# Kernel tuning notes

Hardware: AMD Instinct MI355X
Metric: run time of the kernel (lower is better)

## Reference

```python
import jax, jax.numpy as jnp
import numpy as np

NUM_TAGS = 64
SEQ_LEN = 512
BATCH = 512


def setup_inputs() -> dict:
    key = jax.random.key(0)
    k1, k2, k3, k4, k5 = jax.random.split(key, 5)
    emissions = jax.random.normal(k1, (SEQ_LEN, BATCH, NUM_TAGS), dtype=jnp.float32)
    tags = jax.random.randint(k2, (SEQ_LEN, BATCH), 0, NUM_TAGS, dtype=jnp.int32)
    mask = jnp.ones((SEQ_LEN, BATCH), dtype=jnp.int32)
    start_transitions = jax.random.uniform(k3, (NUM_TAGS,), dtype=jnp.float32)
    end_transitions = jax.random.uniform(k4, (NUM_TAGS,), dtype=jnp.float32)
    transitions = jax.random.uniform(k5, (NUM_TAGS, NUM_TAGS), dtype=jnp.float32)
    return {
        "emissions": emissions,
        "tags": tags,
        "mask": mask,
        "start_transitions": start_transitions,
        "end_transitions": end_transitions,
        "transitions": transitions,
    }


def _compute_score(emissions, tags, mask, start_transitions, end_transitions, transitions):
    # emissions: (S,B,T), tags/mask: (S,B)
    seq_length, batch_size = tags.shape
    maskf = mask.astype(jnp.float32)
    barange = jnp.arange(batch_size)
    # emission scores for gold tags at every step: (S,B)
    emit = jnp.take_along_axis(emissions, tags[:, :, None], axis=2)[:, :, 0]
    # transition scores between consecutive gold tags: (S-1,B)
    trans = transitions[tags[:-1], tags[1:]]
    score = start_transitions[tags[0]] + emit[0]
    score = score + ((trans + emit[1:]) * maskf[1:]).sum(axis=0)
    seq_ends = mask.astype(jnp.int32).sum(axis=0) - 1  # (B,)
    last_tags = tags[seq_ends, barange]
    score = score + end_transitions[last_tags]
    return score  # (B,)


def _compute_normalizer(emissions, mask, start_transitions, end_transitions, transitions):
    # sequential forward-algorithm scan over time
    score0 = start_transitions + emissions[0]  # (B,T)

    def step(score, inp):
        em, m = inp  # em: (B,T), m: (B,)
        # (B,Tprev,Tnext) logsumexp over Tprev
        next_score = jax.nn.logsumexp(
            score[:, :, None] + transitions[None, :, :] + em[:, None, :], axis=1
        )
        score = jnp.where(m[:, None].astype(bool), next_score, score)
        return score, None

    score, _ = jax.lax.scan(step, score0, (emissions[1:], mask[1:]))
    return jax.nn.logsumexp(score + end_transitions, axis=1)  # (B,)


def reference(emissions, tags, mask, start_transitions, end_transitions, transitions):
    numerator = _compute_score(emissions, tags, mask, start_transitions, end_transitions, transitions)
    denominator = _compute_normalizer(emissions, mask, start_transitions, end_transitions, transitions)
    llh = numerator - denominator
    return llh.sum()  # reduction='sum'
```

## Files before the change

### kernel.cpp

```cpp
#include <hip/hip_runtime.h>

#define T   512
#define B   512
#define NT  64
#define QS  16
#define NQ  (T / QS)
#define RING 4

typedef _Float16 h2 __attribute__((ext_vector_type(2)));

__device__ __forceinline__ float rflf(float x) {
    return __uint_as_float(__builtin_amdgcn_readfirstlane(__float_as_uint(x)));
}

__device__ __forceinline__ float dot2(h2 a, h2 b, float c) {
#if __has_builtin(__builtin_amdgcn_fdot2)
    return __builtin_amdgcn_fdot2(a, b, c, false);
#else
    return c + (float)a.x * (float)b.x + (float)a.y * (float)b.y;
#endif
}

__device__ __forceinline__ h2 bch2(int u) { return __builtin_bit_cast(h2, u); }

__global__ __launch_bounds__(64) void crf_fused(
    const float* __restrict__ emissions,
    const int*   __restrict__ tags,
    const int*   __restrict__ mask,
    const float* __restrict__ startT,
    const float* __restrict__ endT,
    const float* __restrict__ trans,
    float* __restrict__ out)
{
    const int j = threadIdx.x;

    __shared__ __align__(16) float ebuf[RING][QS][NT];

    if (blockIdx.x < B) {
        const int b = blockIdx.x;

        h2 Eh[NT / 2];
#pragma unroll
        for (int m = 0; m < NT / 2; ++m) {
            Eh[m].x = (_Float16)__expf(trans[(2 * m)     * NT + j]);
            Eh[m].y = (_Float16)__expf(trans[(2 * m + 1) * NT + j]);
        }

        const int jr = j >> 4;
        const int c0 = (j & 15) * 4;
        float4 sA[4];

        auto issue_q = [&](int g) {
#pragma unroll
            for (int k = 0; k < 4; ++k) {
                const int t = g * QS + 4 * k + jr;
                sA[k] = *(const float4*)&emissions[((size_t)t * B + b) * NT + c0];
            }
        };
        auto write_q = [&](int g) {
#pragma unroll
            for (int k = 0; k < 4; ++k) {
                float4 w;
                w.x = __expf(sA[k].x); w.y = __expf(sA[k].y);
                w.z = __expf(sA[k].z); w.w = __expf(sA[k].w);
                *(float4*)&ebuf[g & (RING - 1)][4 * k + jr][c0] = w;
            }
        };

        for (int g = 0; g < 3; ++g) { issue_q(g); write_q(g); }
        issue_q(3);

        const float e0  = emissions[(size_t)b * NT + j];
        const float sc0 = startT[j] + e0;
        const float S0  = rflf(sc0);
        float q = __expf(sc0 - S0);
        int   K = 0;

        int pk_i;
        {
            const int qi = __float_as_int(q);
            const int qo = __builtin_amdgcn_update_dpp(0, qi, 0xB1, 0xF, 0xF, true);
            pk_i = __builtin_bit_cast(int,
                    __builtin_amdgcn_cvt_pkrtz(q, __int_as_float(qo)));
        }

        float* eflat = &ebuf[0][0][0];
        int bits_prev;
        int mpre = mask[j * B + b];
        unsigned long long mbc = 0;

        {
            int u[32];
#pragma unroll
            for (int n = 0; n < 32; ++n)
                u[n] = __builtin_amdgcn_readlane(pk_i, 2 * n);
            float a[8] = {0.f, 0.f, 0.f, 0.f, 0.f, 0.f, 0.f, 0.f};
#pragma unroll
            for (int n = 0; n < 32; ++n)
                a[n & 7] = dot2(bch2(u[n]), Eh[n], a[n & 7]);
            const float p = ((a[0] + a[1]) + (a[2] + a[3]))
                          + ((a[4] + a[5]) + (a[6] + a[7]));
            bits_prev = __builtin_amdgcn_readfirstlane(__float_as_int(p));
            const int  k = ((bits_prev >> 23) & 255) - 127;
            const float r = __int_as_float((125 - k) << 23);
            const float X1 = eflat[NT + j];
            const int  m1 = mask[B + b];
            if (m1) { q = (p * X1) * r; K = k + 2; }
            const int qo = __builtin_amdgcn_update_dpp(0, __float_as_int(q),
                                                       0xB1, 0xF, 0xF, true);
            pk_i = __builtin_bit_cast(int,
                    __builtin_amdgcn_cvt_pkrtz(q, __int_as_float(qo)));
        }

        float Xc = eflat[2 * NT + j];
        float Xn = eflat[3 * NT + j];

        auto stepF = [&](int s) {
            int u[32];
#pragma unroll
            for (int n = 0; n < 32; ++n)
                u[n] = __builtin_amdgcn_readlane(pk_i, 2 * n);
            __builtin_amdgcn_sched_barrier(0);
            const int  k = ((bits_prev >> 23) & 255) - 127;
            const float r = __int_as_float((125 - k) << 23);
            K += k + 2;
            float a[8] = {0.f, 0.f, 0.f, 0.f, 0.f, 0.f, 0.f, 0.f};
#pragma unroll
            for (int n = 0; n < 32; ++n)
                a[n & 7] = dot2(bch2(u[n]), Eh[n], a[n & 7]);
            const float sXr = Xc * r;
            const float p = ((a[0] + a[1]) + (a[2] + a[3]))
                          + ((a[4] + a[5]) + (a[6] + a[7]));
            q = p * sXr;
            bits_prev = __builtin_amdgcn_readfirstlane(__float_as_int(p));
            const int qo = __builtin_amdgcn_update_dpp(0, __float_as_int(q),
                                                       0xB1, 0xF, 0xF, true);
            pk_i = __builtin_bit_cast(int,
                    __builtin_amdgcn_cvt_pkrtz(q, __int_as_float(qo)));
            Xc = Xn;
            Xn = eflat[((s + 2) & 63) * NT + j];
        };

        auto stepM = [&](int s) {
            int u[32];
#pragma unroll
            for (int n = 0; n < 32; ++n)
                u[n] = __builtin_amdgcn_readlane(pk_i, 2 * n);
            __builtin_amdgcn_sched_barrier(0);
            const int  k = ((bits_prev >> 23) & 255) - 127;
            const float r = __int_as_float((125 - k) << 23);
            const bool mc = (mbc >> (s & 63)) & 1ull;
            const float mf = mc ? 1.0f : 0.0f;
            K += mc ? (k + 2) : 0;
            float a[8] = {0.f, 0.f, 0.f, 0.f, 0.f, 0.f, 0.f, 0.f};
#pragma unroll
            for (int n = 0; n < 32; ++n)
                a[n & 7] = dot2(bch2(u[n]), Eh[n], a[n & 7]);
            const float sXr = Xc * r;
            const float p = ((a[0] + a[1]) + (a[2] + a[3]))
                          + ((a[4] + a[5]) + (a[6] + a[7]));
            const float qn = p * sXr;
            q = fmaf(mf, qn - q, q);
            bits_prev = __builtin_amdgcn_readfirstlane(__float_as_int(p));
            const int qo = __builtin_amdgcn_update_dpp(0, __float_as_int(q),
                                                       0xB1, 0xF, 0xF, true);
            pk_i = __builtin_bit_cast(int,
                    __builtin_amdgcn_cvt_pkrtz(q, __int_as_float(qo)));
            Xc = Xn;
            Xn = eflat[((s + 2) & 63) * NT + j];
        };

        for (int x = 0; x < NQ; ++x) {
            const int gw = (x + 3 < NQ) ? x + 3 : NQ - 1;
            write_q(gw);
            const int gl = (x + 4 < NQ) ? x + 4 : NQ - 1;
            issue_q(gl);

            if ((x & 3) == 0) {
                mbc = __ballot(mpre != 0);
                const int cn = ((x >> 2) + 1 < 8) ? (x >> 2) + 1 : 7;
                mpre = mask[(cn * 64 + j) * B + b];
            }

            const unsigned qb = (unsigned)(mbc >> ((x & 3) << 4)) & 0xFFFFu;
            const int tt0 = (x == 0) ? 2 : 0;

            if (qb == 0xFFFFu) {
#pragma unroll 1
                for (int tt = tt0; tt < QS; ++tt) stepF(x * QS + tt);
            } else {
#pragma unroll 1
                for (int tt = tt0; tt < QS; ++tt) stepM(x * QS + tt);
            }
        }

        float v = q * __expf(endT[j]);
#pragma unroll
        for (int off = 32; off > 0; off >>= 1)
            v += __shfl_xor(v, off);
        if (j == 0)
            atomicAdd(out, -(S0 + (float)K * 0.69314718f + __logf(v)));

    } else {
        const int b = blockIdx.x - B;

        float acc = 0.f;
        int   cnt = 0;
#pragma unroll
        for (int m = 0; m < T / 64; ++m) {
            const int t  = j + 64 * m;
            const int mv = mask[t * B + b];
            const int tg = tags[t * B + b];
            cnt += (int)__popcll(__ballot(mv != 0));
            if (t == 0) {
                acc += startT[tg] + emissions[(size_t)b * NT + tg];
            } else if (mv) {
                const int tp = tags[(t - 1) * B + b];
                acc += trans[tp * NT + tg]
                     + emissions[(size_t)(t * B + b) * NT + tg];
            }
        }
#pragma unroll
        for (int off = 32; off > 0; off >>= 1)
            acc += __shfl_xor(acc, off);
        if (j == 0) {
            const int last = tags[(size_t)(cnt - 1) * B + b];
            atomicAdd(out, acc + endT[last]);
        }
    }
}

extern "C" void kernel_launch(void* const* d_in, const int* in_sizes, int n_in,
                              void* d_out, int out_size, void* d_ws, size_t ws_size,
                              hipStream_t stream) {
    const float* emissions = (const float*)d_in[0];
    const int*   tags      = (const int*)  d_in[1];
    const int*   mask      = (const int*)  d_in[2];
    const float* startT    = (const float*)d_in[3];
    const float* endT      = (const float*)d_in[4];
    const float* trans     = (const float*)d_in[5];
    float* out = (float*)d_out;

    hipMemsetAsync(out, 0, sizeof(float), stream);
    crf_fused<<<2 * B, 64, 0, stream>>>(
        emissions, tags, mask, startT, endT, trans, out);
}
```

Measured before the change: 193.4 us.

## Parallelize forward scan by precomputing per-chunk transfer matrices with MFMA

Splits the 512-step sequential forward recursion into 8 chunks per batch element. A new kernel builds each chunk's 64x64 product of scaled transition-times-emission matrices with fp16 MFMA, storing it and a power-of-two exponent in workspace. A second kernel then applies the 8 chunk matrices sequentially per batch element. This shortens the serial dependency chain and exposes 4096 parallel blocks, at the cost of roughly 33 MB of workspace traffic, extra matrix-matrix work and more fp16 rounding over longer products. The old fused kernel is kept as a fallback when the workspace is missing or too small.

```diff
diff --git a/kernel.cpp b/kernel.cpp
--- a/kernel.cpp
+++ b/kernel.cpp
@@ -3,11 +3,16 @@
 #define T   512
 #define B   512
 #define NT  64
+#define NC  8
+#define CS  64
 #define QS  16
 #define NQ  (T / QS)
 #define RING 4
 
 typedef _Float16 h2 __attribute__((ext_vector_type(2)));
+typedef _Float16 h8 __attribute__((ext_vector_type(8)));
+typedef float   f16x __attribute__((ext_vector_type(16)));
+typedef unsigned int uint;
 
 __device__ __forceinline__ float rflf(float x) {
     return __uint_as_float(__builtin_amdgcn_readfirstlane(__float_as_uint(x)));
@@ -23,52 +28,169 @@
 
 __device__ __forceinline__ h2 bch2(int u) { return __builtin_bit_cast(h2, u); }
 
-__global__ __launch_bounds__(64) void crf_fused(
+__device__ __forceinline__ int cvtpk(float a, float b) {
+    return __builtin_bit_cast(int, __builtin_amdgcn_cvt_pkrtz(a, b));
+}
+
+__global__ __launch_bounds__(64) void crf_chunks(
+    const float* __restrict__ emissions,
+    const int*   __restrict__ mask,
+    const float* __restrict__ trans,
+    uint* __restrict__ wsA,
+    int*  __restrict__ wsK)
+{
+    const int l   = threadIdx.x;
+    const int bc  = blockIdx.x;
+    const int b   = bc >> 3;
+    const int c   = bc & 7;
+    const int col = l & 31;
+    const int hi  = l >> 5;
+
+    __shared__ __align__(16) float xs[CS][NT];
+
+    const int t0 = c * CS;
+    {
+        const int rr = l >> 4;
+        const int cc = (l & 15) * 4;
+#pragma unroll
+        for (int p = 0; p < 16; ++p) {
+            const int tt = p * 4 + rr;
+            float4 v = *(const float4*)&emissions[((size_t)(t0 + tt) * B + b) * NT + cc];
+            float4 w;
+            w.x = __expf(v.x); w.y = __expf(v.y);
+            w.z = __expf(v.z); w.w = __expf(v.w);
+            *(float4*)&xs[tt][cc] = w;
+        }
+    }
+    const unsigned long long mbc = __ballot(mask[(t0 + l) * B + b] != 0);
+
+    h2 Ac[2][4][4];
+#pragma unroll
+    for (int to = 0; to < 2; ++to)
+#pragma unroll
+        for (int ks = 0; ks < 4; ++ks)
+#pragma unroll
+            for (int r = 0; r < 4; ++r) {
+                const int k = ks * 16 + 8 * hi + 2 * r;
+                const int m = to * 32 + col;
+                h2 e;
+                e.x = (_Float16)__expf(trans[k * NT + m]);
+                e.y = (_Float16)__expf(trans[(k + 1) * NT + m]);
+                Ac[to][ks][r] = e;
+            }
+
+    h2 Sb[4][2][4];
+#pragma unroll
+    for (int ks = 0; ks < 4; ++ks)
+#pragma unroll
+        for (int tj = 0; tj < 2; ++tj)
+#pragma unroll
+            for (int r = 0; r < 4; ++r) {
+                const int k = ks * 16 + 8 * hi + 2 * r;
+                const int n = col + 32 * tj;
+                h2 e;
+                e.x = (k     == n) ? (_Float16)1.f : (_Float16)0.f;
+                e.y = (k + 1 == n) ? (_Float16)1.f : (_Float16)0.f;
+                Sb[ks][tj][r] = e;
+            }
+
+    __syncthreads();
+
+    const int paddr = (l ^ 32) << 2;
+    int Kc = 0;
+    int kp = -6;
+    const int sBeg = (c == 0) ? 1 : 0;
+
+#pragma unroll 1
+    for (int tt = sBeg; tt < CS; ++tt) {
+        if (!((mbc >> tt) & 1ull)) continue;
+
+        const float sc = __int_as_float((127 - kp - 6) << 23);
+        Kc += kp + 6;
+        const float x0 = xs[tt][col]      * sc;
+        const float x1 = xs[tt][col + 32] * sc;
+        const h2 X0 = bch2(cvtpk(x0, x0));
+        const h2 X1 = bch2(cvtpk(x1, x1));
+
+        f16x c00 = {}, c01 = {}, c10 = {}, c11 = {};
+#pragma unroll
+        for (int ks = 0; ks < 4; ++ks) {
+            union { h2 p[4]; h8 v; } a0, a1, b0, b1;
+#pragma unroll
+            for (int r = 0; r < 4; ++r) {
+                a0.p[r] = Ac[0][ks][r] * X0;
+                a1.p[r] = Ac[1][ks][r] * X1;
+                b0.p[r] = Sb[ks][0][r];
+                b1.p[r] = Sb[ks][1][r];
+            }
+            c00 = __builtin_amdgcn_mfma_f32_32x32x16_f16(a0.v, b0.v, c00, 0, 0, 0);
+            c01 = __builtin_amdgcn_mfma_f32_32x32x16_f16(a0.v, b1.v, c01, 0, 0, 0);
+            c10 = __builtin_amdgcn_mfma_f32_32x32x16_f16(a1.v, b0.v, c10, 0, 0, 0);
+            c11 = __builtin_amdgcn_mfma_f32_32x32x16_f16(a1.v, b1.v, c11, 0, 0, 0);
+        }
+
+        kp = ((__builtin_amdgcn_readfirstlane(__float_as_int(c00[0])) >> 23) & 255) - 127;
+
+        auto conv = [&](const f16x& A16, int to, int tj) {
+#pragma unroll
+            for (int h = 0; h < 2; ++h) {
+                const int base = 8 * h;
+                const int w0 = cvtpk(A16[base + 0], A16[base + 1]);
+                const int w1 = cvtpk(A16[base + 2], A16[base + 3]);
+                const int w2 = cvtpk(A16[base + 4], A16[base + 5]);
+                const int w3 = cvtpk(A16[base + 6], A16[base + 7]);
+                const int za  = hi ? w0 : w2;
+                const int zb  = hi ? w1 : w3;
+                const int zza = __builtin_amdgcn_ds_bpermute(paddr, za);
+                const int zzb = __builtin_amdgcn_ds_bpermute(paddr, zb);
+                const int ks = 2 * to + h;
+                Sb[ks][tj][0] = bch2(hi ? zza : w0);
+                Sb[ks][tj][1] = bch2(hi ? zzb : w1);
+                Sb[ks][tj][2] = bch2(hi ? w2 : zza);
+                Sb[ks][tj][3] = bch2(hi ? w3 : zzb);
+            }
+        };
+        conv(c00, 0, 0); conv(c01, 0, 1); conv(c10, 1, 0); conv(c11, 1, 1);
+    }
+
+    const uint rowbase = (uint)(bc << 6);
+#pragma unroll
+    for (int ks = 0; ks < 4; ++ks)
+#pragma unroll
+        for (int tj = 0; tj < 2; ++tj)
+#pragma unroll
+            for (int r = 0; r < 4; ++r) {
+                const int w  = __builtin_bit_cast(int, Sb[ks][tj][r]);
+                const int nb = __builtin_amdgcn_update_dpp(0, w, 0xB1, 0xF, 0xF, true);
+                const int n  = col + 32 * tj;
+                uint word; int j;
+                if (l & 1) {
+                    word = ((uint)nb >> 16) | ((uint)w & 0xFFFF0000u);
+                    j = ks * 16 + 8 * hi + 2 * r + 1;
+                } else {
+                    word = ((uint)w & 0xFFFFu) | ((uint)nb << 16);
+                    j = ks * 16 + 8 * hi + 2 * r;
+                }
+                wsA[((size_t)(rowbase + j) << 5) + (n >> 1)] = word;
+            }
+    if (l == 0) wsK[bc] = Kc;
+}
+
+__global__ __launch_bounds__(64) void crf_apply(
     const float* __restrict__ emissions,
     const int*   __restrict__ tags,
     const int*   __restrict__ mask,
     const float* __restrict__ startT,
     const float* __restrict__ endT,
     const float* __restrict__ trans,
+    const uint* __restrict__ wsA,
+    const int*  __restrict__ wsK,
     float* __restrict__ out)
 {
     const int j = threadIdx.x;
 
-    __shared__ __align__(16) float ebuf[RING][QS][NT];
-
     if (blockIdx.x < B) {
         const int b = blockIdx.x;
-
-        h2 Eh[NT / 2];
-#pragma unroll
-        for (int m = 0; m < NT / 2; ++m) {
-            Eh[m].x = (_Float16)__expf(trans[(2 * m)     * NT + j]);
-            Eh[m].y = (_Float16)__expf(trans[(2 * m + 1) * NT + j]);
-        }
-
-        const int jr = j >> 4;
-        const int c0 = (j & 15) * 4;
-        float4 sA[4];
-
-        auto issue_q = [&](int g) {
-#pragma unroll
-            for (int k = 0; k < 4; ++k) {
-                const int t = g * QS + 4 * k + jr;
-                sA[k] = *(const float4*)&emissions[((size_t)t * B + b) * NT + c0];
-            }
-        };
-        auto write_q = [&](int g) {
-#pragma unroll
-            for (int k = 0; k < 4; ++k) {
-                float4 w;
-                w.x = __expf(sA[k].x); w.y = __expf(sA[k].y);
-                w.z = __expf(sA[k].z); w.w = __expf(sA[k].w);
-                *(float4*)&ebuf[g & (RING - 1)][4 * k + jr][c0] = w;
-            }
-        };
-
-        for (int g = 0; g < 3; ++g) { issue_q(g); write_q(g); }
-        issue_q(3);
 
         const float e0  = emissions[(size_t)b * NT + j];
         const float sc0 = startT[j] + e0;
@@ -76,122 +198,44 @@
         float q = __expf(sc0 - S0);
         int   K = 0;
 
-        int pk_i;
-        {
+#pragma unroll 1
+        for (int c = 0; c < NC; ++c) {
+            const int bc = b * NC + c;
+            const int4* ap = (const int4*)(wsA + ((size_t)(bc * 64 + j) << 5));
+            union { int4 q4[8]; int w[32]; } A;
+#pragma unroll
+            for (int m = 0; m < 8; ++m) A.q4[m] = ap[m];
+            const int Kc = wsK[bc];
+
             const int qi = __float_as_int(q);
             const int qo = __builtin_amdgcn_update_dpp(0, qi, 0xB1, 0xF, 0xF, true);
-            pk_i = __builtin_bit_cast(int,
-                    __builtin_amdgcn_cvt_pkrtz(q, __int_as_float(qo)));
-        }
-
-        float* eflat = &ebuf[0][0][0];
-        int bits_prev;
-        int mpre = mask[j * B + b];
-        unsigned long long mbc = 0;
-
-        {
-            int u[32];
-#pragma unroll
-            for (int n = 0; n < 32; ++n)
-                u[n] = __builtin_amdgcn_readlane(pk_i, 2 * n);
-            float a[8] = {0.f, 0.f, 0.f, 0.f, 0.f, 0.f, 0.f, 0.f};
-#pragma unroll
-            for (int n = 0; n < 32; ++n)
-                a[n & 7] = dot2(bch2(u[n]), Eh[n], a[n & 7]);
-            const float p = ((a[0] + a[1]) + (a[2] + a[3]))
-                          + ((a[4] + a[5]) + (a[6] + a[7]));
-            bits_prev = __builtin_amdgcn_readfirstlane(__float_as_int(p));
-            const int  k = ((bits_prev >> 23) & 255) - 127;
-            const float r = __int_as_float((125 - k) << 23);
-            const float X1 = eflat[NT + j];
-            const int  m1 = mask[B + b];
-            if (m1) { q = (p * X1) * r; K = k + 2; }
-            const int qo = __builtin_amdgcn_update_dpp(0, __float_as_int(q),
-                                                       0xB1, 0xF, 0xF, true);
-            pk_i = __builtin_bit_cast(int,
-                    __builtin_amdgcn_cvt_pkrtz(q, __int_as_float(qo)));
-        }
-
-        float Xc = eflat[2 * NT + j];
-        float Xn = eflat[3 * NT + j];
-
-        auto stepF = [&](int s) {
-            int u[32];
-#pragma unroll
-            for (int n = 0; n < 32; ++n)
-                u[n] = __builtin_amdgcn_readlane(pk_i, 2 * n);
-            __builtin_amdgcn_sched_barrier(0);
-            const int  k = ((bits_prev >> 23) & 255) - 127;
-            const float r = __int_as_float((125 - k) << 23);
-            K += k + 2;
-            float a[8] = {0.f, 0.f, 0.f, 0.f, 0.f, 0.f, 0.f, 0.f};
-#pragma unroll
-            for (int n = 0; n < 32; ++n)
-                a[n & 7] = dot2(bch2(u[n]), Eh[n], a[n & 7]);
-            const float sXr = Xc * r;
-            const float p = ((a[0] + a[1]) + (a[2] + a[3]))
-                          + ((a[4] + a[5]) + (a[6] + a[7]));
-            q = p * sXr;
-            bits_prev = __builtin_amdgcn_readfirstlane(__float_as_int(p));
-            const int qo = __builtin_amdgcn_update_dpp(0, __float_as_int(q),
-                                                       0xB1, 0xF, 0xF, true);
-            pk_i = __builtin_bit_cast(int,
-                    __builtin_amdgcn_cvt_pkrtz(q, __int_as_float(qo)));
-            Xc = Xn;
-            Xn = eflat[((s + 2) & 63) * NT + j];
-        };
-
-        auto stepM = [&](int s) {
-            int u[32];
-#pragma unroll
-            for (int n = 0; n < 32; ++n)
-                u[n] = __builtin_amdgcn_readlane(pk_i, 2 * n);
-            __builtin_amdgcn_sched_barrier(0);
-            const int  k = ((bits_prev >> 23) & 255) - 127;
-            const float r = __int_as_float((125 - k) << 23);
-            const bool mc = (mbc >> (s & 63)) & 1ull;
-            const float mf = mc ? 1.0f : 0.0f;
-            K += mc ? (k + 2) : 0;
-            float a[8] = {0.f, 0.f, 0.f, 0.f, 0.f, 0.f, 0.f, 0.f};
-#pragma unroll
-            for (int n = 0; n < 32; ++n)
-                a[n & 7] = dot2(bch2(u[n]), Eh[n], a[n & 7]);
-            const float sXr = Xc * r;
-            const float p = ((a[0] + a[1]) + (a[2] + a[3]))
-                          + ((a[4] + a[5]) + (a[6] + a[7]));
-            const float qn = p * sXr;
-            q = fmaf(mf, qn - q, q);
-            bits_prev = __builtin_amdgcn_readfirstlane(__float_as_int(p));
-            const int qo = __builtin_amdgcn_update_dpp(0, __float_as_int(q),
-                                                       0xB1, 0xF, 0xF, true);
-            pk_i = __builtin_bit_cast(int,
-                    __builtin_amdgcn_cvt_pkrtz(q, __int_as_float(qo)));
-            Xc = Xn;
-            Xn = eflat[((s + 2) & 63) * NT + j];
-        };
-
-        for (int x = 0; x < NQ; ++x) {
-            const int gw = (x + 3 < NQ) ? x + 3 : NQ - 1;
-            write_q(gw);
-            const int gl = (x + 4 < NQ) ? x + 4 : NQ - 1;
-            issue_q(gl);
-
-            if ((x & 3) == 0) {
-                mbc = __ballot(mpre != 0);
-                const int cn = ((x >> 2) + 1 < 8) ? (x >> 2) + 1 : 7;
-                mpre = mask[(cn * 64 + j) * B + b];
-            }
-
-            const unsigned qb = (unsigned)(mbc >> ((x & 3) << 4)) & 0xFFFFu;
-            const int tt0 = (x == 0) ? 2 : 0;
-
-            if (qb == 0xFFFFu) {
-#pragma unroll 1
-                for (int tt = tt0; tt < QS; ++tt) stepF(x * QS + tt);
-            } else {
-#pragma unroll 1
-                for (int tt = tt0; tt < QS; ++tt) stepM(x * QS + tt);
-            }
+            const int pk = cvtpk(q, __int_as_float(qo));
+
+            float a0 = 0.f, a1 = 0.f, a2 = 0.f, a3 = 0.f;
+            float a4 = 0.f, a5 = 0.f, a6 = 0.f, a7 = 0.f;
+#pragma unroll
+            for (int n = 0; n < 4; ++n) {
+                int u[8];
+#pragma unroll
+                for (int m = 0; m < 8; ++m)
+                    u[m] = __builtin_amdgcn_readlane(pk, 16 * n + 2 * m);
+                const int e = 8 * n;
+                a0 = dot2(bch2(u[0]), bch2(A.w[e + 0]), a0);
+                a1 = dot2(bch2(u[1]), bch2(A.w[e + 1]), a1);
+                a2 = dot2(bch2(u[2]), bch2(A.w[e + 2]), a2);
+                a3 = dot2(bch2(u[3]), bch2(A.w[e + 3]), a3);
+                a4 = dot2(bch2(u[4]), bch2(A.w[e + 4]), a4);
+                a5 = dot2(bch2(u[5]), bch2(A.w[e + 5]), a5);
+                a6 = dot2(bch2(u[6]), bch2(A.w[e + 6]), a6);
+                a7 = dot2(bch2(u[7]), bch2(A.w[e + 7]), a7);
+            }
+            const float p = ((a0 + a1) + (a2 + a3)) + ((a4 + a5) + (a6 + a7));
+
+            const int bits = __builtin_amdgcn_readfirstlane(__float_as_int(p));
+            const int k    = ((bits >> 23) & 255) - 127;
+            const float r  = __int_as_float((127 - k) << 23);
+            q = p * r;
+            K += k + Kc;
         }
 
         float v = q * __expf(endT[j]);
@@ -230,6 +274,176 @@
     }
 }
 
+__global__ __launch_bounds__(64) void crf_fused(
+    const float* __restrict__ emissions,
+    const int*   __restrict__ tags,
+    const int*   __restrict__ mask,
+    const float* __restrict__ startT,
+    const float* __restrict__ endT,
+    const float* __restrict__ trans,
+    float* __restrict__ out)
+{
+    const int j = threadIdx.x;
+    __shared__ __align__(16) float ebuf[RING][QS][NT];
+
+    if (blockIdx.x < B) {
+        const int b = blockIdx.x;
+        h2 Eh[NT / 2];
+#pragma unroll
+        for (int m = 0; m < NT / 2; ++m) {
+            Eh[m].x = (_Float16)__expf(trans[(2 * m)     * NT + j]);
+            Eh[m].y = (_Float16)__expf(trans[(2 * m + 1) * NT + j]);
+        }
+        const int jr = j >> 4;
+        const int c0 = (j & 15) * 4;
+        float4 sA[4];
+        auto issue_q = [&](int g) {
+#pragma unroll
+            for (int k = 0; k < 4; ++k) {
+                const int t = g * QS + 4 * k + jr;
+                sA[k] = *(const float4*)&emissions[((size_t)t * B + b) * NT + c0];
+            }
+        };
+        auto write_q = [&](int g) {
+#pragma unroll
+            for (int k = 0; k < 4; ++k) {
+                float4 w;
+                w.x = __expf(sA[k].x); w.y = __expf(sA[k].y);
+                w.z = __expf(sA[k].z); w.w = __expf(sA[k].w);
+                *(float4*)&ebuf[g & (RING - 1)][4 * k + jr][c0] = w;
+            }
+        };
+        for (int g = 0; g < 3; ++g) { issue_q(g); write_q(g); }
+        issue_q(3);
+
+        const float e0  = emissions[(size_t)b * NT + j];
+        const float sc0 = startT[j] + e0;
+        const float S0  = rflf(sc0);
+        float q = __expf(sc0 - S0);
+        int   K = 0;
+        int pk_i;
+        {
+            const int qi = __float_as_int(q);
+            const int qo = __builtin_amdgcn_update_dpp(0, qi, 0xB1, 0xF, 0xF, true);
+            pk_i = cvtpk(q, __int_as_float(qo));
+        }
+        float* eflat = &ebuf[0][0][0];
+        int bits_prev;
+        int mpre = mask[j * B + b];
+        unsigned long long mbc = 0;
+        {
+            int u[32];
+#pragma unroll
+            for (int n = 0; n < 32; ++n) u[n] = __builtin_amdgcn_readlane(pk_i, 2 * n);
+            float a[8] = {0.f,0.f,0.f,0.f,0.f,0.f,0.f,0.f};
+#pragma unroll
+            for (int n = 0; n < 32; ++n) a[n & 7] = dot2(bch2(u[n]), Eh[n], a[n & 7]);
+            const float p = ((a[0]+a[1])+(a[2]+a[3])) + ((a[4]+a[5])+(a[6]+a[7]));
+            bits_prev = __builtin_amdgcn_readfirstlane(__float_as_int(p));
+            const int  k = ((bits_prev >> 23) & 255) - 127;
+            const float r = __int_as_float((125 - k) << 23);
+            const float X1 = eflat[NT + j];
+            const int  m1 = mask[B + b];
+            if (m1) { q = (p * X1) * r; K = k + 2; }
+            const int qo = __builtin_amdgcn_update_dpp(0, __float_as_int(q), 0xB1, 0xF, 0xF, true);
+            pk_i = cvtpk(q, __int_as_float(qo));
+        }
+        float Xc = eflat[2 * NT + j];
+        float Xn = eflat[3 * NT + j];
+        auto stepF = [&](int s) {
+            int u[32];
+#pragma unroll
+            for (int n = 0; n < 32; ++n) u[n] = __builtin_amdgcn_readlane(pk_i, 2 * n);
+            __builtin_amdgcn_sched_barrier(0);
+            const int  k = ((bits_prev >> 23) & 255) - 127;
+            const float r = __int_as_float((125 - k) << 23);
+            K += k + 2;
+            float a[8] = {0.f,0.f,0.f,0.f,0.f,0.f,0.f,0.f};
+#pragma unroll
+            for (int n = 0; n < 32; ++n) a[n & 7] = dot2(bch2(u[n]), Eh[n], a[n & 7]);
+            const float sXr = Xc * r;
+            const float p = ((a[0]+a[1])+(a[2]+a[3])) + ((a[4]+a[5])+(a[6]+a[7]));
+            q = p * sXr;
+            bits_prev = __builtin_amdgcn_readfirstlane(__float_as_int(p));
+            const int qo = __builtin_amdgcn_update_dpp(0, __float_as_int(q), 0xB1, 0xF, 0xF, true);
+            pk_i = cvtpk(q, __int_as_float(qo));
+            Xc = Xn;
+            Xn = eflat[((s + 2) & 63) * NT + j];
+        };
+        auto stepM = [&](int s) {
+            int u[32];
+#pragma unroll
+            for (int n = 0; n < 32; ++n) u[n] = __builtin_amdgcn_readlane(pk_i, 2 * n);
+            __builtin_amdgcn_sched_barrier(0);
+            const int  k = ((bits_prev >> 23) & 255) - 127;
+            const float r = __int_as_float((125 - k) << 23);
+            const bool mc = (mbc >> (s & 63)) & 1ull;
+            const float mf = mc ? 1.0f : 0.0f;
+            K += mc ? (k + 2) : 0;
+            float a[8] = {0.f,0.f,0.f,0.f,0.f,0.f,0.f,0.f};
+#pragma unroll
+            for (int n = 0; n < 32; ++n) a[n & 7] = dot2(bch2(u[n]), Eh[n], a[n & 7]);
+            const float sXr = Xc * r;
+            const float p = ((a[0]+a[1])+(a[2]+a[3])) + ((a[4]+a[5])+(a[6]+a[7]));
+            const float qn = p * sXr;
+            q = fmaf(mf, qn - q, q);
+            bits_prev = __builtin_amdgcn_readfirstlane(__float_as_int(p));
+            const int qo = __builtin_amdgcn_update_dpp(0, __float_as_int(q), 0xB1, 0xF, 0xF, true);
+            pk_i = cvtpk(q, __int_as_float(qo));
+            Xc = Xn;
+            Xn = eflat[((s + 2) & 63) * NT + j];
+        };
+        for (int x = 0; x < NQ; ++x) {
+            const int gw = (x + 3 < NQ) ? x + 3 : NQ - 1;
+            write_q(gw);
+            const int gl = (x + 4 < NQ) ? x + 4 : NQ - 1;
+            issue_q(gl);
+            if ((x & 3) == 0) {
+                mbc = __ballot(mpre != 0);
+                const int cn = ((x >> 2) + 1 < 8) ? (x >> 2) + 1 : 7;
+                mpre = mask[(cn * 64 + j) * B + b];
+            }
+            const unsigned qb = (unsigned)(mbc >> ((x & 3) << 4)) & 0xFFFFu;
+            const int tt0 = (x == 0) ? 2 : 0;
+            if (qb == 0xFFFFu) {
+#pragma unroll 1
+                for (int tt = tt0; tt < QS; ++tt) stepF(x * QS + tt);
+            } else {
+#pragma unroll 1
+                for (int tt = tt0; tt < QS; ++tt) stepM(x * QS + tt);
+            }
+        }
+        float v = q * __expf(endT[j]);
+#pragma unroll
+        for (int off = 32; off > 0; off >>= 1) v += __shfl_xor(v, off);
+        if (j == 0)
+            atomicAdd(out, -(S0 + (float)K * 0.69314718f + __logf(v)));
+    } else {
+        const int b = blockIdx.x - B;
+        float acc = 0.f;
+        int   cnt = 0;
+#pragma unroll
+        for (int m = 0; m < T / 64; ++m) {
+            const int t  = j + 64 * m;
+            const int mv = mask[t * B + b];
+            const int tg = tags[t * B + b];
+            cnt += (int)__popcll(__ballot(mv != 0));
+            if (t == 0) {
+                acc += startT[tg] + emissions[(size_t)b * NT + tg];
+            } else if (mv) {
+                const int tp = tags[(t - 1) * B + b];
+                acc += trans[tp * NT + tg] + emissions[(size_t)(t * B + b) * NT + tg];
+            }
+        }
+#pragma unroll
+        for (int off = 32; off > 0; off >>= 1) acc += __shfl_xor(acc, off);
+        if (j == 0) {
+            const int last = tags[(size_t)(cnt - 1) * B + b];
+            atomicAdd(out, acc + endT[last]);
+        }
+    }
+}
+
 extern "C" void kernel_launch(void* const* d_in, const int* in_sizes, int n_in,
                               void* d_out, int out_size, void* d_ws, size_t ws_size,
                               hipStream_t stream) {
@@ -242,6 +456,17 @@
     float* out = (float*)d_out;
 
     hipMemsetAsync(out, 0, sizeof(float), stream);
-    crf_fused<<<2 * B, 64, 0, stream>>>(
-        emissions, tags, mask, startT, endT, trans, out);
-}
+
+    const size_t needA = (size_t)B * NC * 64 * 32 * sizeof(uint);
+    const size_t need  = needA + (size_t)B * NC * sizeof(int);
+    if (d_ws != nullptr && ws_size >= need) {
+        uint* wsA = (uint*)d_ws;
+        int*  wsK = (int*)((char*)d_ws + needA);
+        crf_chunks<<<B * NC, 64, 0, stream>>>(emissions, mask, trans, wsA, wsK);
+        crf_apply<<<2 * B, 64, 0, stream>>>(emissions, tags, mask, startT, endT,
+                                            trans, wsA, wsK, out);
+    } else {
+        crf_fused<<<2 * B, 64, 0, stream>>>(emissions, tags, mask, startT, endT,
+                                            trans, out);
+    }
+}
```

New measurement: 276.0 us. 1.43x slower.

## Batch 16 sequences per wave with MFMA forward step and prepacked fp16 emissions

Applied to the files above, without the earlier changes.

Adds a prep kernel that exponentiates emissions and packs them to fp16 into a workspace in an MFMA-friendly layout, and also computes the gold-path scores. The new step kernel processes 16 batch elements per wave and does the 64x64 transition product with 16x16x32 fp16 MFMAs instead of per-lane dot2 over readlane broadcasts. It rescales with a shared exponent plus a periodic per-column fp16 renormalization. The aim is to cut the per-step broadcast and dot cost, but only 32 waves run the sequential scan, and the fp16 state risks range and precision loss. The old fused kernel remains as a fallback when the workspace is too small.

```diff
diff --git a/kernel.cpp b/kernel.cpp
--- a/kernel.cpp
+++ b/kernel.cpp
@@ -8,10 +8,18 @@
 #define RING 4
 
 typedef _Float16 h2 __attribute__((ext_vector_type(2)));
+typedef _Float16 h8 __attribute__((ext_vector_type(8)));
+typedef float    f4 __attribute__((ext_vector_type(4)));
+typedef unsigned int uint;
 
 __device__ __forceinline__ float rflf(float x) {
     return __uint_as_float(__builtin_amdgcn_readfirstlane(__float_as_uint(x)));
 }
+__device__ __forceinline__ int cvtpk(float a, float b) {
+    return __builtin_bit_cast(int, __builtin_amdgcn_cvt_pkrtz(a, b));
+}
+__device__ __forceinline__ h2  bch2(int u) { return __builtin_bit_cast(h2, u); }
+__device__ __forceinline__ int bci(h2 u)   { return __builtin_bit_cast(int, u); }
 
 __device__ __forceinline__ float dot2(h2 a, h2 b, float c) {
 #if __has_builtin(__builtin_amdgcn_fdot2)
@@ -21,7 +29,206 @@
 #endif
 }
 
-__device__ __forceinline__ h2 bch2(int u) { return __builtin_bit_cast(h2, u); }
+__global__ __launch_bounds__(256) void crf_prep(
+    const float* __restrict__ emissions,
+    const int*   __restrict__ tags,
+    const int*   __restrict__ mask,
+    const float* __restrict__ startT,
+    const float* __restrict__ endT,
+    const float* __restrict__ trans,
+    uint4* __restrict__ xp,
+    float* __restrict__ out)
+{
+    if (blockIdx.x < 8192) {
+        const int lin = blockIdx.x * 256 + threadIdx.x;
+        const int l  = lin & 63;
+        const int h  = (lin >> 6) & 1;
+        const int wv = (lin >> 7) & 31;
+        const int t  = lin >> 12;
+        const int b  = wv * 16 + (l & 15);
+        const int g  = l >> 4;
+        const float* p = &emissions[((size_t)t * B + b) * NT + 32 * h + 8 * g];
+        const float4 v0 = *(const float4*)p;
+        const float4 v1 = *(const float4*)(p + 4);
+        uint4 w;
+        w.x = (uint)cvtpk(__expf(v0.x), __expf(v0.y));
+        w.y = (uint)cvtpk(__expf(v0.z), __expf(v0.w));
+        w.z = (uint)cvtpk(__expf(v1.x), __expf(v1.y));
+        w.w = (uint)cvtpk(__expf(v1.z), __expf(v1.w));
+        xp[lin] = w;
+    } else {
+        const int l  = threadIdx.x & 63;
+        const int b  = (blockIdx.x - 8192) * 4 + (threadIdx.x >> 6);
+        float acc = 0.f;
+        int   cnt = 0;
+#pragma unroll
+        for (int m = 0; m < T / 64; ++m) {
+            const int t  = l + 64 * m;
+            const int mv = mask[t * B + b];
+            const int tg = tags[t * B + b];
+            cnt += (int)__popcll(__ballot(mv != 0));
+            if (t == 0) {
+                acc += startT[tg] + emissions[(size_t)b * NT + tg];
+            } else if (mv) {
+                const int tp = tags[(t - 1) * B + b];
+                acc += trans[tp * NT + tg]
+                     + emissions[(size_t)(t * B + b) * NT + tg];
+            }
+        }
+#pragma unroll
+        for (int off = 32; off > 0; off >>= 1)
+            acc += __shfl_xor(acc, off);
+        if (l == 0) {
+            const int last = tags[(size_t)(cnt - 1) * B + b];
+            atomicAdd(out, acc + endT[last]);
+        }
+    }
+}
+
+__global__ __launch_bounds__(64) void crf_step(
+    const float* __restrict__ emissions,
+    const int*   __restrict__ mask,
+    const float* __restrict__ startT,
+    const float* __restrict__ endT,
+    const float* __restrict__ trans,
+    const uint4* __restrict__ xp,
+    float* __restrict__ out)
+{
+    const int l  = threadIdx.x;
+    const int wv = blockIdx.x;
+    const int n  = l & 15;
+    const int g  = l >> 4;
+    const int b  = wv * 16 + n;
+
+    union AH { _Float16 e[8]; h8 v; };
+    AH A[4][2];
+#pragma unroll
+    for (int rho = 0; rho < 4; ++rho)
+#pragma unroll
+        for (int c = 0; c < 2; ++c)
+#pragma unroll
+            for (int e = 0; e < 8; ++e) {
+                const int k = 32 * c + 8 * g + e;
+                const int j = 32 * (rho >> 1) + 4 * (rho & 1)
+                            + 8 * (n >> 2) + (n & 3);
+                A[rho][c].e[e] = (_Float16)__expf(trans[k * NT + j]);
+            }
+
+    const float S0 = startT[0] + emissions[(size_t)b * NT];
+    int QW[8];
+    {
+        const float* e0 = &emissions[(size_t)b * NT];
+#pragma unroll
+        for (int w = 0; w < 8; ++w) {
+            const int tb = 32 * (w >> 2) + 8 * g + 2 * (w & 3);
+            const float v0 = __expf(startT[tb]     + e0[tb]     - S0);
+            const float v1 = __expf(startT[tb + 1] + e0[tb + 1] - S0);
+            QW[w] = cvtpk(v0, v1);
+        }
+    }
+    int K = 0;
+
+    uint4 pfa[4], pfb[4];
+    int   pfm[4];
+    auto PF = [&](int t, int slot) {
+        const int tc = t < T ? t : T - 1;
+        const uint4* xb = xp + (size_t)(tc * 32 + wv) * 128 + l;
+        pfa[slot] = xb[0];
+        pfb[slot] = xb[64];
+        pfm[slot] = mask[tc * B + b];
+    };
+    PF(1, 1); PF(2, 2); PF(3, 3); PF(4, 0);
+
+    const f4 z4 = {0.f, 0.f, 0.f, 0.f};
+
+#pragma unroll 1
+    for (int base = 1; base < 512; base += 4) {
+#pragma unroll
+        for (int u = 0; u < 4; ++u) {
+            const int t = base + u;
+            if (t < 512) {
+                const int slot = (1 + u) & 3;
+                const uint4 xlo = pfa[slot];
+                const uint4 xhi = pfb[slot];
+                const int   mv  = pfm[slot];
+                PF(t + 4, slot);
+
+                union HB { int w[4]; h8 v; };
+                HB b0, b1;
+                b0.w[0] = QW[0]; b0.w[1] = QW[1]; b0.w[2] = QW[2]; b0.w[3] = QW[3];
+                b1.w[0] = QW[4]; b1.w[1] = QW[5]; b1.w[2] = QW[6]; b1.w[3] = QW[7];
+
+                f4 c0 = __builtin_amdgcn_mfma_f32_16x16x32_f16(A[0][0].v, b0.v, z4, 0, 0, 0);
+                f4 c1 = __builtin_amdgcn_mfma_f32_16x16x32_f16(A[1][0].v, b0.v, z4, 0, 0, 0);
+                f4 c2 = __builtin_amdgcn_mfma_f32_16x16x32_f16(A[2][0].v, b0.v, z4, 0, 0, 0);
+                f4 c3 = __builtin_amdgcn_mfma_f32_16x16x32_f16(A[3][0].v, b0.v, z4, 0, 0, 0);
+                c0 = __builtin_amdgcn_mfma_f32_16x16x32_f16(A[0][1].v, b1.v, c0, 0, 0, 0);
+                c1 = __builtin_amdgcn_mfma_f32_16x16x32_f16(A[1][1].v, b1.v, c1, 0, 0, 0);
+                c2 = __builtin_amdgcn_mfma_f32_16x16x32_f16(A[2][1].v, b1.v, c2, 0, 0, 0);
+                c3 = __builtin_amdgcn_mfma_f32_16x16x32_f16(A[3][1].v, b1.v, c3, 0, 0, 0);
+
+                const int bits = __builtin_amdgcn_readfirstlane(__float_as_int(c0[0]));
+                const int kw   = ((bits >> 23) & 255) - 127;
+                const int sb   = (kw + 2) << 23;
+
+                auto cw = [&](float a, float bb2) {
+                    return cvtpk(__int_as_float(__float_as_int(a)   - sb),
+                                 __int_as_float(__float_as_int(bb2) - sb));
+                };
+                int nw[8];
+                nw[0] = bci(bch2(cw(c0[0], c0[1])) * bch2((int)xlo.x));
+                nw[1] = bci(bch2(cw(c0[2], c0[3])) * bch2((int)xlo.y));
+                nw[2] = bci(bch2(cw(c1[0], c1[1])) * bch2((int)xlo.z));
+                nw[3] = bci(bch2(cw(c1[2], c1[3])) * bch2((int)xlo.w));
+                nw[4] = bci(bch2(cw(c2[0], c2[1])) * bch2((int)xhi.x));
+                nw[5] = bci(bch2(cw(c2[2], c2[3])) * bch2((int)xhi.y));
+                nw[6] = bci(bch2(cw(c3[0], c3[1])) * bch2((int)xhi.z));
+                nw[7] = bci(bch2(cw(c3[2], c3[3])) * bch2((int)xhi.w));
+
+                const bool mc = mv != 0;
+                if (__ballot(mc) == ~0ull) {
+#pragma unroll
+                    for (int w = 0; w < 8; ++w) QW[w] = nw[w];
+                    K += kw + 2;
+                } else {
+#pragma unroll
+                    for (int w = 0; w < 8; ++w) QW[w] = mc ? nw[w] : QW[w];
+                    K += mc ? (kw + 2) : 0;
+                }
+
+                if (u == 3) {
+                    const int rep = __builtin_amdgcn_ds_bpermute(n << 2, QW[0]);
+                    const int d   = ((rep >> 10) & 31) - 15;
+                    int se = 13 - d;
+                    se = se < 1 ? 1 : (se > 30 ? 30 : se);
+                    const int sw = (se << 10) | (se << 26);
+#pragma unroll
+                    for (int w = 0; w < 8; ++w)
+                        QW[w] = bci(bch2(QW[w]) * bch2(sw));
+                    K += 15 - se;
+                }
+            }
+        }
+    }
+
+    float v = 0.f;
+#pragma unroll
+    for (int w = 0; w < 8; ++w) {
+        const int tb = 32 * (w >> 2) + 8 * g + 2 * (w & 3);
+        const h2 qq = bch2(QW[w]);
+        v += (float)qq.x * __expf(endT[tb]);
+        v += (float)qq.y * __expf(endT[tb + 1]);
+    }
+    v += __shfl_xor(v, 16);
+    v += __shfl_xor(v, 32);
+    float con = 0.f;
+    if (l < 16)
+        con = -(S0 + (float)K * 0.69314718f + __logf(v));
+#pragma unroll
+    for (int off = 32; off > 0; off >>= 1)
+        con += __shfl_xor(con, off);
+    if (l == 0) atomicAdd(out, con);
+}
 
 __global__ __launch_bounds__(64) void crf_fused(
     const float* __restrict__ emissions,
@@ -33,23 +240,19 @@
     float* __restrict__ out)
 {
     const int j = threadIdx.x;
-
     __shared__ __align__(16) float ebuf[RING][QS][NT];
 
     if (blockIdx.x < B) {
         const int b = blockIdx.x;
-
         h2 Eh[NT / 2];
 #pragma unroll
         for (int m = 0; m < NT / 2; ++m) {
             Eh[m].x = (_Float16)__expf(trans[(2 * m)     * NT + j]);
             Eh[m].y = (_Float16)__expf(trans[(2 * m + 1) * NT + j]);
         }
-
         const int jr = j >> 4;
         const int c0 = (j & 15) * 4;
         float4 sA[4];
-
         auto issue_q = [&](int g) {
 #pragma unroll
             for (int k = 0; k < 4; ++k) {
@@ -66,7 +269,6 @@
                 *(float4*)&ebuf[g & (RING - 1)][4 * k + jr][c0] = w;
             }
         };
-
         for (int g = 0; g < 3; ++g) { issue_q(g); write_q(g); }
         issue_q(3);
 
@@ -75,116 +277,90 @@
         const float S0  = rflf(sc0);
         float q = __expf(sc0 - S0);
         int   K = 0;
-
         int pk_i;
         {
             const int qi = __float_as_int(q);
             const int qo = __builtin_amdgcn_update_dpp(0, qi, 0xB1, 0xF, 0xF, true);
-            pk_i = __builtin_bit_cast(int,
-                    __builtin_amdgcn_cvt_pkrtz(q, __int_as_float(qo)));
-        }
-
+            pk_i = cvtpk(q, __int_as_float(qo));
+        }
         float* eflat = &ebuf[0][0][0];
         int bits_prev;
         int mpre = mask[j * B + b];
         unsigned long long mbc = 0;
-
         {
             int u[32];
 #pragma unroll
-            for (int n = 0; n < 32; ++n)
-                u[n] = __builtin_amdgcn_readlane(pk_i, 2 * n);
-            float a[8] = {0.f, 0.f, 0.f, 0.f, 0.f, 0.f, 0.f, 0.f};
-#pragma unroll
-            for (int n = 0; n < 32; ++n)
-                a[n & 7] = dot2(bch2(u[n]), Eh[n], a[n & 7]);
-            const float p = ((a[0] + a[1]) + (a[2] + a[3]))
-                          + ((a[4] + a[5]) + (a[6] + a[7]));
+            for (int m = 0; m < 32; ++m) u[m] = __builtin_amdgcn_readlane(pk_i, 2 * m);
+            float a[8] = {0.f,0.f,0.f,0.f,0.f,0.f,0.f,0.f};
+#pragma unroll
+            for (int m = 0; m < 32; ++m) a[m & 7] = dot2(bch2(u[m]), Eh[m], a[m & 7]);
+            const float p = ((a[0]+a[1])+(a[2]+a[3])) + ((a[4]+a[5])+(a[6]+a[7]));
             bits_prev = __builtin_amdgcn_readfirstlane(__float_as_int(p));
             const int  k = ((bits_prev >> 23) & 255) - 127;
             const float r = __int_as_float((125 - k) << 23);
             const float X1 = eflat[NT + j];
             const int  m1 = mask[B + b];
             if (m1) { q = (p * X1) * r; K = k + 2; }
-            const int qo = __builtin_amdgcn_update_dpp(0, __float_as_int(q),
-                                                       0xB1, 0xF, 0xF, true);
-            pk_i = __builtin_bit_cast(int,
-                    __builtin_amdgcn_cvt_pkrtz(q, __int_as_float(qo)));
-        }
-
+            const int qo = __builtin_amdgcn_update_dpp(0, __float_as_int(q), 0xB1, 0xF, 0xF, true);
+            pk_i = cvtpk(q, __int_as_float(qo));
+        }
         float Xc = eflat[2 * NT + j];
         float Xn = eflat[3 * NT + j];
-
         auto stepF = [&](int s) {
             int u[32];
 #pragma unroll
-            for (int n = 0; n < 32; ++n)
-                u[n] = __builtin_amdgcn_readlane(pk_i, 2 * n);
+            for (int m = 0; m < 32; ++m) u[m] = __builtin_amdgcn_readlane(pk_i, 2 * m);
             __builtin_amdgcn_sched_barrier(0);
             const int  k = ((bits_prev >> 23) & 255) - 127;
             const float r = __int_as_float((125 - k) << 23);
             K += k + 2;
-            float a[8] = {0.f, 0.f, 0.f, 0.f, 0.f, 0.f, 0.f, 0.f};
-#pragma unroll
-            for (int n = 0; n < 32; ++n)
-                a[n & 7] = dot2(bch2(u[n]), Eh[n], a[n & 7]);
+            float a[8] = {0.f,0.f,0.f,0.f,0.f,0.f,0.f,0.f};
+#pragma unroll
+            for (int m = 0; m < 32; ++m) a[m & 7] = dot2(bch2(u[m]), Eh[m], a[m & 7]);
             const float sXr = Xc * r;
-            const float p = ((a[0] + a[1]) + (a[2] + a[3]))
-                          + ((a[4] + a[5]) + (a[6] + a[7]));
+            const float p = ((a[0]+a[1])+(a[2]+a[3])) + ((a[4]+a[5])+(a[6]+a[7]));
             q = p * sXr;
             bits_prev = __builtin_amdgcn_readfirstlane(__float_as_int(p));
-            const int qo = __builtin_amdgcn_update_dpp(0, __float_as_int(q),
-                                                       0xB1, 0xF, 0xF, true);
-            pk_i = __builtin_bit_cast(int,
-                    __builtin_amdgcn_cvt_pkrtz(q, __int_as_float(qo)));
+            const int qo = __builtin_amdgcn_update_dpp(0, __float_as_int(q), 0xB1, 0xF, 0xF, true);
+            pk_i = cvtpk(q, __int_as_float(qo));
             Xc = Xn;
             Xn = eflat[((s + 2) & 63) * NT + j];
         };
-
         auto stepM = [&](int s) {
             int u[32];
 #pragma unroll
-            for (int n = 0; n < 32; ++n)
-                u[n] = __builtin_amdgcn_readlane(pk_i, 2 * n);
+            for (int m = 0; m < 32; ++m) u[m] = __builtin_amdgcn_readlane(pk_i, 2 * m);
             __builtin_amdgcn_sched_barrier(0);
             const int  k = ((bits_prev >> 23) & 255) - 127;
             const float r = __int_as_float((125 - k) << 23);
             const bool mc = (mbc >> (s & 63)) & 1ull;
             const float mf = mc ? 1.0f : 0.0f;
             K += mc ? (k + 2) : 0;
-            float a[8] = {0.f, 0.f, 0.f, 0.f, 0.f, 0.f, 0.f, 0.f};
-#pragma unroll
-            for (int n = 0; n < 32; ++n)
-                a[n & 7] = dot2(bch2(u[n]), Eh[n], a[n & 7]);
+            float a[8] = {0.f,0.f,0.f,0.f,0.f,0.f,0.f,0.f};
+#pragma unroll
+            for (int m = 0; m < 32; ++m) a[m & 7] = dot2(bch2(u[m]), Eh[m], a[m & 7]);
             const float sXr = Xc * r;
-            const float p = ((a[0] + a[1]) + (a[2] + a[3]))
-                          + ((a[4] + a[5]) + (a[6] + a[7]));
+            const float p = ((a[0]+a[1])+(a[2]+a[3])) + ((a[4]+a[5])+(a[6]+a[7]));
             const float qn = p * sXr;
             q = fmaf(mf, qn - q, q);
             bits_prev = __builtin_amdgcn_readfirstlane(__float_as_int(p));
-            const int qo = __builtin_amdgcn_update_dpp(0, __float_as_int(q),
-                                                       0xB1, 0xF, 0xF, true);
-            pk_i = __builtin_bit_cast(int,
-                    __builtin_amdgcn_cvt_pkrtz(q, __int_as_float(qo)));
+            const int qo = __builtin_amdgcn_update_dpp(0, __float_as_int(q), 0xB1, 0xF, 0xF, true);
+            pk_i = cvtpk(q, __int_as_float(qo));
             Xc = Xn;
             Xn = eflat[((s + 2) & 63) * NT + j];
         };
-
         for (int x = 0; x < NQ; ++x) {
             const int gw = (x + 3 < NQ) ? x + 3 : NQ - 1;
             write_q(gw);
             const int gl = (x + 4 < NQ) ? x + 4 : NQ - 1;
             issue_q(gl);
-
             if ((x & 3) == 0) {
                 mbc = __ballot(mpre != 0);
                 const int cn = ((x >> 2) + 1 < 8) ? (x >> 2) + 1 : 7;
                 mpre = mask[(cn * 64 + j) * B + b];
             }
-
             const unsigned qb = (unsigned)(mbc >> ((x & 3) << 4)) & 0xFFFFu;
             const int tt0 = (x == 0) ? 2 : 0;
-
             if (qb == 0xFFFFu) {
 #pragma unroll 1
                 for (int tt = tt0; tt < QS; ++tt) stepF(x * QS + tt);
@@ -193,17 +369,13 @@
                 for (int tt = tt0; tt < QS; ++tt) stepM(x * QS + tt);
             }
         }
-
         float v = q * __expf(endT[j]);
 #pragma unroll
-        for (int off = 32; off > 0; off >>= 1)
-            v += __shfl_xor(v, off);
+        for (int off = 32; off > 0; off >>= 1) v += __shfl_xor(v, off);
         if (j == 0)
             atomicAdd(out, -(S0 + (float)K * 0.69314718f + __logf(v)));
-
     } else {
         const int b = blockIdx.x - B;
-
         float acc = 0.f;
         int   cnt = 0;
 #pragma unroll
@@ -216,13 +388,11 @@
                 acc += startT[tg] + emissions[(size_t)b * NT + tg];
             } else if (mv) {
                 const int tp = tags[(t - 1) * B + b];
-                acc += trans[tp * NT + tg]
-                     + emissions[(size_t)(t * B + b) * NT + tg];
-            }
-        }
-#pragma unroll
-        for (int off = 32; off > 0; off >>= 1)
-            acc += __shfl_xor(acc, off);
+                acc += trans[tp * NT + tg] + emissions[(size_t)(t * B + b) * NT + tg];
+            }
+        }
+#pragma unroll
+        for (int off = 32; off > 0; off >>= 1) acc += __shfl_xor(acc, off);
         if (j == 0) {
             const int last = tags[(size_t)(cnt - 1) * B + b];
             atomicAdd(out, acc + endT[last]);
@@ -242,6 +412,16 @@
     float* out = (float*)d_out;
 
     hipMemsetAsync(out, 0, sizeof(float), stream);
-    crf_fused<<<2 * B, 64, 0, stream>>>(
-        emissions, tags, mask, startT, endT, trans, out);
-}
+
+    const size_t need = (size_t)8192 * 256 * 16;
+    if (d_ws != nullptr && ws_size >= need) {
+        uint4* xp = (uint4*)d_ws;
+        crf_prep<<<8192 + 128, 256, 0, stream>>>(emissions, tags, mask,
+                                                 startT, endT, trans, xp, out);
+        crf_step<<<32, 64, 0, stream>>>(emissions, mask, startT, endT, trans,
+                                        xp, out);
+    } else {
+        crf_fused<<<2 * B, 64, 0, stream>>>(emissions, tags, mask, startT,
+                                            endT, trans, out);
+    }
+}
```

New measurement: 247.5 us. 28.0% more time.
